# Kernel optimization log

Measured on AMD Instinct MI355X. Metric: run time of the kernel, lower is better.

## Reference

```python
import jax, jax.numpy as jnp
import numpy as np

N, C_IN, C_OUT = 8192, 128, 128
BN_EPS = 1e-5
EDGE_PROB = 0.004  # avg degree ~33


def setup_inputs() -> dict:
    key = jax.random.key(0)
    k1, k2, k3, k4, k5, k6 = jax.random.split(key, 6)
    node_features = jax.random.normal(k1, (N, C_IN), dtype=jnp.float32)
    # binary dense adjacency (rand fill, thresholded to ~avg degree 33)
    adjacency_matrix = (jax.random.uniform(k2, (N, N)) < EDGE_PROB).astype(jnp.float32)
    s = 1.0 / np.sqrt(C_IN)
    W_n = jax.random.uniform(k3, (C_OUT, C_IN), jnp.float32, -s, s)
    b_n = jax.random.uniform(k4, (C_OUT,), jnp.float32, -s, s)
    W_c = jax.random.uniform(k5, (C_OUT, C_IN), jnp.float32, -s, s)
    b_c = jax.random.uniform(k6, (C_OUT,), jnp.float32, -s, s)
    gamma = jnp.ones((C_OUT,), jnp.float32)
    beta = jnp.zeros((C_OUT,), jnp.float32)
    return {"node_features": node_features, "adjacency_matrix": adjacency_matrix,
            "W_n": W_n, "b_n": b_n, "W_c": W_c, "b_c": b_c,
            "gamma": gamma, "beta": beta}


def reference(node_features, adjacency_matrix, W_n, b_n, W_c, b_c, gamma, beta):
    # mean aggregation: degrees from row-sums (as in the torch code), agg = A.T @ X / deg
    deg = adjacency_matrix.sum(axis=1, keepdims=True)          # [N,1]
    deg = jnp.where(deg == 0, jnp.ones_like(deg), deg)
    agg = (adjacency_matrix.T @ node_features) / deg           # [N,C_in]
    h = agg @ W_n.T + b_n + node_features @ W_c.T + b_c        # [N,C_out]
    # BatchNorm1d, training-mode batch stats (biased variance)
    mu = h.mean(axis=0)
    var = ((h - mu) ** 2).mean(axis=0)
    h_norm = (h - mu) * jax.lax.rsqrt(var + BN_EPS)
    return jax.nn.relu(gamma * h_norm + beta)
```

## Files before the change

kernel.cpp:

```cpp
#include <hip/hip_runtime.h>
#include <stdint.h>

#define NN 8192
#define CC 128
#define BN_EPS 1e-5f

__device__ inline unsigned short f2bf(float f) {
    unsigned int u = __float_as_uint(f);
    unsigned int r = (u + 0x7fffu + ((u >> 16) & 1u)) >> 16;
    return (unsigned short)r;
}
__device__ inline float bf2f(unsigned short s) {
    return __uint_as_float(((unsigned int)s) << 16);
}

__device__ __forceinline__ void process_pair(
        float4 a, float xa0, float xb0, float xa1, float xb1,
        int j0, float* __restrict__ acc, float* __restrict__ deg, int lane) {
    unsigned long long m0 = __ballot(a.x != 0.0f);
    unsigned long long m1 = __ballot(a.y != 0.0f);
    unsigned long long m2 = __ballot(a.z != 0.0f);
    unsigned long long m3 = __ballot(a.w != 0.0f);
    if ((m0 | m1 | m2 | m3) == 0ull) return;
    const unsigned long long LO = 0xffffffffull;
    int c0 = __popcll(m0 & LO) + __popcll(m1 & LO) + __popcll(m2 & LO) + __popcll(m3 & LO);
    int c1 = __popcll(m0 >> 32) + __popcll(m1 >> 32) + __popcll(m2 >> 32) + __popcll(m3 >> 32);
    if (lane == 0 && c0) atomicAdd(&deg[j0], (float)c0);
    if (lane == 1 && c1) atomicAdd(&deg[j0 + 1], (float)c1);
    unsigned long long m[4] = {m0, m1, m2, m3};
    #pragma unroll
    for (int comp = 0; comp < 4; ++comp) {
        unsigned int lo = (unsigned int)m[comp];
        while (lo) {
            int b = __builtin_ctz(lo); lo &= lo - 1;
            int il = 4 * b + comp;
            atomicAdd(&acc[il * 128 + lane],      xa0);
            atomicAdd(&acc[il * 128 + 64 + lane], xb0);
        }
        unsigned int hi = (unsigned int)(m[comp] >> 32);
        while (hi) {
            int b = __builtin_ctz(hi); hi &= hi - 1;
            int il = 4 * b + comp;
            atomicAdd(&acc[il * 128 + lane],      xa1);
            atomicAdd(&acc[il * 128 + 64 + lane], xb1);
        }
    }
}

#define LOADB(a_, xa_, xb_, j0_) do {                                          \
    const float* Ap_ = A + (size_t)((j0_) + (lane >> 5)) * NN + i0 + ((lane & 31) << 2); \
    _Pragma("unroll")                                                          \
    for (int u = 0; u < 4; ++u)                                                \
        a_[u] = *reinterpret_cast<const float4*>(Ap_ + (size_t)(2 * u) * NN);  \
    _Pragma("unroll")                                                          \
    for (int r = 0; r < 8; ++r) {                                              \
        xa_[r] = X[((j0_) + r) * CC + lane];                                   \
        xb_[r] = X[((j0_) + r) * CC + 64 + lane];                              \
    }                                                                          \
} while (0)

#define PROCB(a_, xa_, xb_, j0_) do {                                          \
    _Pragma("unroll")                                                          \
    for (int u = 0; u < 4; ++u)                                                \
        process_pair(a_[u], xa_[2 * u], xb_[2 * u], xa_[2 * u + 1],            \
                     xb_[2 * u + 1], (j0_) + 2 * u, acc, deg, lane);           \
} while (0)

__global__ __launch_bounds__(256, 2) void k1_spmm(
        const float* __restrict__ A, const float* __restrict__ X,
        float* __restrict__ aggU, float* __restrict__ deg) {
    __shared__ float acc[128 * 128];
    const int tid  = threadIdx.x;
    const int lane = tid & 63;
    const int wave = tid >> 6;
    const int i0   = blockIdx.x * 128;
    const int jbase = blockIdx.y * 1024 + wave * 256;

    for (int t = tid; t < 128 * 128; t += 256) acc[t] = 0.0f;
    __syncthreads();

    float4 a0[4], a1[4];
    float xa0[8], xb0[8], xa1[8], xb1[8];

    LOADB(a0, xa0, xb0, jbase);
    for (int it2 = 0; it2 < 16; ++it2) {
        int j0 = jbase + it2 * 16;
        LOADB(a1, xa1, xb1, j0 + 8);
        PROCB(a0, xa0, xb0, j0);
        if (it2 < 15) LOADB(a0, xa0, xb0, j0 + 16);
        PROCB(a1, xa1, xb1, j0 + 8);
    }

    __syncthreads();
    float* aggBase = aggU + (size_t)i0 * CC;
    for (int t = tid; t < 128 * 128; t += 256) atomicAdd(&aggBase[t], acc[t]);
}

__global__ __launch_bounds__(256, 2) void k2_gemm(
        const float* __restrict__ aggU, const float* __restrict__ deg,
        const float* __restrict__ X,
        const float* __restrict__ Wn, const float* __restrict__ bn,
        const float* __restrict__ Wc, const float* __restrict__ bc,
        float* __restrict__ h, float* __restrict__ bsum, float* __restrict__ bsq) {
    __shared__ unsigned short WtN[128 * 128];
    __shared__ unsigned short WtC[128 * 128];
    const int tid = threadIdx.x;
    for (int idx = tid * 4; idx < 128 * 128; idx += 1024) {
        float4 wn4 = *reinterpret_cast<const float4*>(Wn + idx);
        float4 wc4 = *reinterpret_cast<const float4*>(Wc + idx);
        int c = idx >> 7, k0 = idx & 127;
        WtN[(k0 + 0) * 128 + c] = f2bf(wn4.x);
        WtN[(k0 + 1) * 128 + c] = f2bf(wn4.y);
        WtN[(k0 + 2) * 128 + c] = f2bf(wn4.z);
        WtN[(k0 + 3) * 128 + c] = f2bf(wn4.w);
        WtC[(k0 + 0) * 128 + c] = f2bf(wc4.x);
        WtC[(k0 + 1) * 128 + c] = f2bf(wc4.y);
        WtC[(k0 + 2) * 128 + c] = f2bf(wc4.z);
        WtC[(k0 + 3) * 128 + c] = f2bf(wc4.w);
    }
    __syncthreads();
    const int c  = tid & 127;
    const int rg = tid >> 7;
    const int i0 = blockIdx.x * 16 + rg * 8;

    float accN[8], accC[8];
    #pragma unroll
    for (int r = 0; r < 8; ++r) { accN[r] = 0.0f; accC[r] = 0.0f; }

    float4 ar[8], xr[8], an[8], xn[8];

#define LOADK(ab_, xb_, k_) do {                                               \
    _Pragma("unroll")                                                          \
    for (int r = 0; r < 8; ++r) {                                              \
        ab_[r] = *reinterpret_cast<const float4*>(&aggU[(size_t)(i0 + r) * CC + (k_)]); \
        xb_[r] = *reinterpret_cast<const float4*>(&X[(size_t)(i0 + r) * CC + (k_)]);    \
    }                                                                          \
} while (0)

#define COMPK(ab_, xb_, k_) do {                                               \
    _Pragma("unroll")                                                          \
    for (int kk = 0; kk < 4; ++kk) {                                           \
        float wn_ = bf2f(WtN[((k_) + kk) * 128 + c]);                          \
        float wc_ = bf2f(WtC[((k_) + kk) * 128 + c]);                          \
        _Pragma("unroll")                                                      \
        for (int r = 0; r < 8; ++r) {                                          \
            accN[r] = fmaf((&ab_[r].x)[kk], wn_, accN[r]);                     \
            accC[r] = fmaf((&xb_[r].x)[kk], wc_, accC[r]);                     \
        }                                                                      \
    }                                                                          \
} while (0)

    LOADK(ar, xr, 0);
    for (int k = 0; k < 128; k += 8) {
        LOADK(an, xn, k + 4);
        COMPK(ar, xr, k);
        if (k + 8 < 128) LOADK(ar, xr, k + 8);
        COMPK(an, xn, k + 4);
    }

    const float bnc = bn[c], bcc = bc[c];
    float sp = 0.0f, sq = 0.0f;
    #pragma unroll
    for (int r = 0; r < 8; ++r) {
        float d  = deg[i0 + r];
        float rd = (d == 0.0f) ? 1.0f : (1.0f / d);
        float hv = accN[r] * rd + accC[r] + bnc + bcc;
        h[(size_t)(i0 + r) * CC + c] = hv;
        sp += hv; sq += hv * hv;
    }
    __syncthreads();
    float* red = reinterpret_cast<float*>(WtN);
    red[rg * 128 + c]       = sp;
    red[256 + rg * 128 + c] = sq;
    __syncthreads();
    if (rg == 0) {
        atomicAdd(&bsum[c], red[c] + red[128 + c]);
        atomicAdd(&bsq[c],  red[256 + c] + red[384 + c]);
    }
}

__global__ __launch_bounds__(256) void k4_bn(
        const float* __restrict__ h, const float* __restrict__ bsum,
        const float* __restrict__ bsq, const float* __restrict__ gamma,
        const float* __restrict__ beta, float* __restrict__ out) {
    const int idx = (blockIdx.x * 256 + threadIdx.x) * 4;
    const int c0  = idx & 127;
    float4 hv = *reinterpret_cast<const float4*>(h + idx);
    float4 s4 = *reinterpret_cast<const float4*>(bsum + c0);
    float4 q4 = *reinterpret_cast<const float4*>(bsq + c0);
    float4 g4 = *reinterpret_cast<const float4*>(gamma + c0);
    float4 b4 = *reinterpret_cast<const float4*>(beta + c0);
    const float invN = 1.0f / 8192.0f;
    float4 o;
    const float* hp = &hv.x; const float* sp = &s4.x; const float* qp = &q4.x;
    const float* gp = &g4.x; const float* bp = &b4.x; float* op = &o.x;
    #pragma unroll
    for (int jj = 0; jj < 4; ++jj) {
        float mu  = sp[jj] * invN;
        float var = qp[jj] * invN - mu * mu;
        float sc  = gp[jj] * rsqrtf(var + BN_EPS);
        float v   = (hp[jj] - mu) * sc + bp[jj];
        op[jj] = v > 0.0f ? v : 0.0f;
    }
    *reinterpret_cast<float4*>(out + idx) = o;
}

extern "C" void kernel_launch(void* const* d_in, const int* in_sizes, int n_in,
                              void* d_out, int out_size, void* d_ws, size_t ws_size,
                              hipStream_t stream) {
    const float* X     = (const float*)d_in[0];
    const float* A     = (const float*)d_in[1];
    const float* Wn    = (const float*)d_in[2];
    const float* bn    = (const float*)d_in[3];
    const float* Wc    = (const float*)d_in[4];
    const float* bc    = (const float*)d_in[5];
    const float* gamma = (const float*)d_in[6];
    const float* beta  = (const float*)d_in[7];
    float* out = (float*)d_out;

    char* ws = (char*)d_ws;
    float* aggU = (float*)(ws);
    float* deg  = (float*)(ws + 4194304);
    float* bsum = (float*)(ws + 4227072);
    float* bsq  = (float*)(ws + 4227584);
    float* h    = (float*)(ws + 4228096);

    hipMemsetAsync(d_ws, 0, 4228096, stream);

    k1_spmm<<<dim3(64, 8), 256, 0, stream>>>(A, X, aggU, deg);
    k2_gemm<<<512, 256, 0, stream>>>(aggU, deg, X, Wn, bn, Wc, bc, h, bsum, bsq);
    k4_bn<<<1024, 256, 0, stream>>>(h, bsum, bsq, gamma, beta, out);
}
```

Before: 529.1 us.

## Split dense-adjacency SpMM into edge-compaction scan and shared-memory gather kernels

The fused SpMM kernel is replaced by two kernels. The first streams the dense adjacency with nontemporal loads, computes degrees and compacts nonzeros into per-region edge lists through atomic counters. The second gathers X rows only for the recorded edges and accumulates them in shared memory. This removes the per-row X loads and the interleaving of scan and scatter work from the bandwidth-bound pass over A, and spreads the scan over more blocks. In exchange it adds a kernel launch and a fixed per-region capacity that silently drops edges if a 64x128 tile has more than 512 nonzeros. The edge buffer reuses the memory later used for h.

```diff
diff --git a/kernel.cpp b/kernel.cpp
--- a/kernel.cpp
+++ b/kernel.cpp
@@ -4,6 +4,9 @@
 #define NN 8192
 #define CC 128
 #define BN_EPS 1e-5f
+#define REG_CAP 512
+
+typedef float vf4 __attribute__((ext_vector_type(4)));
 
 __device__ inline unsigned short f2bf(float f) {
     unsigned int u = __float_as_uint(f);
@@ -14,86 +17,120 @@
     return __uint_as_float(((unsigned int)s) << 16);
 }
 
-__device__ __forceinline__ void process_pair(
-        float4 a, float xa0, float xb0, float xa1, float xb1,
-        int j0, float* __restrict__ acc, float* __restrict__ deg, int lane) {
-    unsigned long long m0 = __ballot(a.x != 0.0f);
-    unsigned long long m1 = __ballot(a.y != 0.0f);
-    unsigned long long m2 = __ballot(a.z != 0.0f);
-    unsigned long long m3 = __ballot(a.w != 0.0f);
-    if ((m0 | m1 | m2 | m3) == 0ull) return;
-    const unsigned long long LO = 0xffffffffull;
-    int c0 = __popcll(m0 & LO) + __popcll(m1 & LO) + __popcll(m2 & LO) + __popcll(m3 & LO);
-    int c1 = __popcll(m0 >> 32) + __popcll(m1 >> 32) + __popcll(m2 >> 32) + __popcll(m3 >> 32);
-    if (lane == 0 && c0) atomicAdd(&deg[j0], (float)c0);
-    if (lane == 1 && c1) atomicAdd(&deg[j0 + 1], (float)c1);
-    unsigned long long m[4] = {m0, m1, m2, m3};
-    #pragma unroll
-    for (int comp = 0; comp < 4; ++comp) {
-        unsigned int lo = (unsigned int)m[comp];
-        while (lo) {
-            int b = __builtin_ctz(lo); lo &= lo - 1;
-            int il = 4 * b + comp;
-            atomicAdd(&acc[il * 128 + lane],      xa0);
-            atomicAdd(&acc[il * 128 + 64 + lane], xb0);
-        }
-        unsigned int hi = (unsigned int)(m[comp] >> 32);
-        while (hi) {
-            int b = __builtin_ctz(hi); hi &= hi - 1;
-            int il = 4 * b + comp;
-            atomicAdd(&acc[il * 128 + lane],      xa1);
-            atomicAdd(&acc[il * 128 + 64 + lane], xb1);
-        }
-    }
-}
-
-#define LOADB(a_, xa_, xb_, j0_) do {                                          \
-    const float* Ap_ = A + (size_t)((j0_) + (lane >> 5)) * NN + i0 + ((lane & 31) << 2); \
-    _Pragma("unroll")                                                          \
-    for (int u = 0; u < 4; ++u)                                                \
-        a_[u] = *reinterpret_cast<const float4*>(Ap_ + (size_t)(2 * u) * NN);  \
-    _Pragma("unroll")                                                          \
-    for (int r = 0; r < 8; ++r) {                                              \
-        xa_[r] = X[((j0_) + r) * CC + lane];                                   \
-        xb_[r] = X[((j0_) + r) * CC + 64 + lane];                              \
-    }                                                                          \
-} while (0)
-
-#define PROCB(a_, xa_, xb_, j0_) do {                                          \
-    _Pragma("unroll")                                                          \
-    for (int u = 0; u < 4; ++u)                                                \
-        process_pair(a_[u], xa_[2 * u], xb_[2 * u], xa_[2 * u + 1],            \
-                     xb_[2 * u + 1], (j0_) + 2 * u, acc, deg, lane);           \
-} while (0)
-
-__global__ __launch_bounds__(256, 2) void k1_spmm(
-        const float* __restrict__ A, const float* __restrict__ X,
-        float* __restrict__ aggU, float* __restrict__ deg) {
-    __shared__ float acc[128 * 128];
+__global__ __launch_bounds__(256) void k1_scan(
+        const float* __restrict__ A, float* __restrict__ deg,
+        unsigned* __restrict__ cnt, unsigned* __restrict__ edges) {
     const int tid  = threadIdx.x;
     const int lane = tid & 63;
     const int wave = tid >> 6;
-    const int i0   = blockIdx.x * 128;
-    const int jbase = blockIdx.y * 1024 + wave * 256;
-
+    const int x = blockIdx.x, y = blockIdx.y;
+    const int i0  = x * 128;
+    const int reg = y * 64 + x;
+    unsigned* eb = edges + (size_t)reg * REG_CAP;
+    const int jb0 = y * 256 + wave * 64;
+    const float* Ap = A + (size_t)(jb0 + (lane >> 5)) * NN + i0 + ((lane & 31) << 2);
+    const unsigned long long lt = (1ull << lane) - 1ull;
+
+    auto procb = [&](const vf4* a, int jb) {
+        #pragma unroll
+        for (int u = 0; u < 4; ++u) {
+            vf4 v = a[u];
+            int j0 = jb + 2 * u;
+            unsigned long long m0 = __ballot(v.x != 0.0f);
+            unsigned long long m1 = __ballot(v.y != 0.0f);
+            unsigned long long m2 = __ballot(v.z != 0.0f);
+            unsigned long long m3 = __ballot(v.w != 0.0f);
+            if (!(m0 | m1 | m2 | m3)) continue;
+            int cLo = __popc((unsigned)m0) + __popc((unsigned)m1)
+                    + __popc((unsigned)m2) + __popc((unsigned)m3);
+            int cHi = __popc((unsigned)(m0 >> 32)) + __popc((unsigned)(m1 >> 32))
+                    + __popc((unsigned)(m2 >> 32)) + __popc((unsigned)(m3 >> 32));
+            if (lane == 0 && cLo) atomicAdd(&deg[j0],     (float)cLo);
+            if (lane == 1 && cHi) atomicAdd(&deg[j0 + 1], (float)cHi);
+            unsigned base = 0;
+            if (lane == 0) base = atomicAdd(&cnt[reg], (unsigned)(cLo + cHi));
+            base = (unsigned)__shfl((int)base, 0);
+            int j  = j0 + (lane >> 5);
+            int cb = (lane & 31) << 2;
+            unsigned long long mc[4] = {m0, m1, m2, m3};
+            float vv[4] = {v.x, v.y, v.z, v.w};
+            unsigned pre = base;
+            #pragma unroll
+            for (int c = 0; c < 4; ++c) {
+                if (vv[c] != 0.0f) {
+                    unsigned slot = pre + (unsigned)__popcll(mc[c] & lt);
+                    if (slot < REG_CAP)
+                        eb[slot] = ((unsigned)j << 7) | (unsigned)(cb + c);
+                }
+                pre += (unsigned)__popcll(mc[c]);
+            }
+        }
+    };
+
+#define LD(dst, roff) do { _Pragma("unroll")                                   \
+    for (int u = 0; u < 4; ++u)                                                \
+        dst[u] = __builtin_nontemporal_load(                                   \
+            reinterpret_cast<const vf4*>(Ap + (size_t)((roff) + 2 * u) * NN)); \
+    } while (0)
+
+    vf4 a0[4], a1[4];
+    LD(a0, 0);
+    for (int nI = 0; nI < 4; ++nI) {
+        int r = nI * 16;
+        LD(a1, r + 8);
+        procb(a0, jb0 + r);
+        if (nI < 3) LD(a0, r + 16);
+        procb(a1, jb0 + r + 8);
+    }
+#undef LD
+}
+
+__global__ __launch_bounds__(256, 2) void k1b_gather(
+        const float* __restrict__ X, const unsigned* __restrict__ cnt,
+        const unsigned* __restrict__ edges, float* __restrict__ aggU) {
+    __shared__ float acc[128 * 128];
+    const int tid = threadIdx.x, lane = tid & 63, wave = tid >> 6;
+    const int x = blockIdx.x, yb = blockIdx.y;
     for (int t = tid; t < 128 * 128; t += 256) acc[t] = 0.0f;
     __syncthreads();
-
-    float4 a0[4], a1[4];
-    float xa0[8], xb0[8], xa1[8], xb1[8];
-
-    LOADB(a0, xa0, xb0, jbase);
-    for (int it2 = 0; it2 < 16; ++it2) {
-        int j0 = jbase + it2 * 16;
-        LOADB(a1, xa1, xb1, j0 + 8);
-        PROCB(a0, xa0, xb0, j0);
-        if (it2 < 15) LOADB(a0, xa0, xb0, j0 + 16);
-        PROCB(a1, xa1, xb1, j0 + 8);
-    }
-
-    __syncthreads();
-    float* aggBase = aggU + (size_t)i0 * CC;
-    for (int t = tid; t < 128 * 128; t += 256) atomicAdd(&aggBase[t], acc[t]);
+    const int reg = (yb * 4 + wave) * 64 + x;
+    const unsigned* eb = edges + (size_t)reg * REG_CAP;
+    unsigned n = cnt[reg]; if (n > REG_CAP) n = REG_CAP;
+
+#define LE(e_, t0_) do { _Pragma("unroll")                                     \
+    for (int u = 0; u < 4; ++u) e_[u] = eb[(t0_) + u]; } while (0)
+#define LX(e_, xa_, xb_) do { _Pragma("unroll")                                \
+    for (int u = 0; u < 4; ++u) { int j_ = (int)(e_[u] >> 7);                  \
+        xa_[u] = X[j_ * CC + lane]; xb_[u] = X[j_ * CC + 64 + lane]; } } while (0)
+#define PR(e_, xa_, xb_) do { _Pragma("unroll")                                \
+    for (int u = 0; u < 4; ++u) { int il_ = (int)(e_[u] & 127u);               \
+        atomicAdd(&acc[il_ * 128 + lane],      xa_[u]);                        \
+        atomicAdd(&acc[il_ * 128 + 64 + lane], xb_[u]); } } while (0)
+
+    unsigned e0[4], e1[4];
+    float xa0[4], xb0[4], xa1[4], xb1[4];
+    unsigned base = 0;
+    if (n >= 8) {
+        LE(e0, 0); LX(e0, xa0, xb0);
+        while (base + 8 <= n) {
+            LE(e1, base + 4); LX(e1, xa1, xb1);
+            PR(e0, xa0, xb0);
+            if (base + 12 <= n) { LE(e0, base + 8); LX(e0, xa0, xb0); }
+            PR(e1, xa1, xb1);
+            base += 8;
+        }
+    }
+    for (unsigned s = base; s < n; ++s) {
+        unsigned e = eb[s]; int j = (int)(e >> 7), il = (int)(e & 127u);
+        atomicAdd(&acc[il * 128 + lane],      X[j * CC + lane]);
+        atomicAdd(&acc[il * 128 + 64 + lane], X[j * CC + 64 + lane]);
+    }
+#undef LE
+#undef LX
+#undef PR
+    __syncthreads();
+    float* out = aggU + (size_t)x * 128 * CC;
+    for (int t = tid; t < 128 * 128; t += 256) atomicAdd(&out[t], acc[t]);
 }
 
 __global__ __launch_bounds__(256, 2) void k2_gemm(
@@ -157,6 +194,8 @@
         if (k + 8 < 128) LOADK(ar, xr, k + 8);
         COMPK(an, xn, k + 4);
     }
+#undef LOADK
+#undef COMPK
 
     const float bnc = bn[c], bcc = bc[c];
     float sp = 0.0f, sq = 0.0f;
@@ -219,15 +258,17 @@
     float* out = (float*)d_out;
 
     char* ws = (char*)d_ws;
-    float* aggU = (float*)(ws);
-    float* deg  = (float*)(ws + 4194304);
-    float* bsum = (float*)(ws + 4227072);
-    float* bsq  = (float*)(ws + 4227584);
-    float* h    = (float*)(ws + 4228096);
-
-    hipMemsetAsync(d_ws, 0, 4228096, stream);
-
-    k1_spmm<<<dim3(64, 8), 256, 0, stream>>>(A, X, aggU, deg);
-    k2_gemm<<<512, 256, 0, stream>>>(aggU, deg, X, Wn, bn, Wc, bc, h, bsum, bsq);
-    k4_bn<<<1024, 256, 0, stream>>>(h, bsum, bsq, gamma, beta, out);
-}
+    float*    aggU  = (float*)(ws);
+    float*    deg   = (float*)(ws + 4194304);
+    float*    bsum  = (float*)(ws + 4227072);
+    float*    bsq   = (float*)(ws + 4227584);
+    unsigned* cnt   = (unsigned*)(ws + 4228096);
+    float*    h     = (float*)(ws + 4236288);
+    unsigned* edges = (unsigned*)(ws + 4236288);
+    hipMemsetAsync(d_ws, 0, 4236288, stream);
+
+    k1_scan  <<<dim3(64, 32), 256, 0, stream>>>(A, deg, cnt, edges);
+    k1b_gather<<<dim3(64, 8), 256, 0, stream>>>(X, cnt, edges, aggU);
+    k2_gemm  <<<512, 256, 0, stream>>>(aggU, deg, X, Wn, bn, Wc, bc, h, bsum, bsq);
+    k4_bn    <<<1024, 256, 0, stream>>>(h, bsum, bsq, gamma, beta, out);
+}
```

New measurement: 614.0 us. 16.0% more time.
